# Performance work log

Measured on AMD Instinct MI355X. Metric: run time of the kernel, lower is better.

Reference implementation:

```python
import jax, jax.numpy as jnp
import numpy as np

N = 50000       # nodes
E = 800000      # edges (before self-loops)
F_IN = 128
HID = 64
HEADS = 4
OUT_DIM = 128
N_CLS = 2
NG = 500        # num graphs
SLOPE = 0.2     # GATConv leaky_relu negative slope
EPS = 1e-5      # BatchNorm eps


def setup_inputs() -> dict:
    key = jax.random.key(0)
    ks = jax.random.split(key, 24)
    s = 0.05
    d = {
        "x": jax.random.normal(ks[0], (N, F_IN), jnp.float32),
        "edge_index": jax.random.randint(ks[1], (2, E), 0, N, jnp.int64),
        "batch": jnp.sort(jax.random.randint(ks[2], (N,), 0, NG, jnp.int64)),
        # GATConv 1
        "W1": jax.random.normal(ks[3], (F_IN, HEADS * HID), jnp.float32) * s,
        "att_src1": jax.random.normal(ks[4], (HEADS, HID), jnp.float32) * s,
        "att_dst1": jax.random.normal(ks[5], (HEADS, HID), jnp.float32) * s,
        "b1": jnp.zeros((HEADS * HID,), jnp.float32),
        # BN1 (eval mode)
        "g1": jnp.ones((HEADS * HID,), jnp.float32),
        "be1": jnp.zeros((HEADS * HID,), jnp.float32),
        "rm1": jnp.zeros((HEADS * HID,), jnp.float32),
        "rv1": jnp.ones((HEADS * HID,), jnp.float32),
        # GATConv 2
        "W2": jax.random.normal(ks[6], (HEADS * HID, HEADS * HID), jnp.float32) * s,
        "att_src2": jax.random.normal(ks[7], (HEADS, HID), jnp.float32) * s,
        "att_dst2": jax.random.normal(ks[8], (HEADS, HID), jnp.float32) * s,
        "b2": jnp.zeros((HEADS * HID,), jnp.float32),
        # BN2 (eval mode)
        "g2": jnp.ones((HEADS * HID,), jnp.float32),
        "be2": jnp.zeros((HEADS * HID,), jnp.float32),
        "rm2": jnp.zeros((HEADS * HID,), jnp.float32),
        "rv2": jnp.ones((HEADS * HID,), jnp.float32),
        # MLP head
        "lw1": jax.random.normal(ks[9], (HEADS * HID, OUT_DIM), jnp.float32) * s,
        "lb1": jnp.zeros((OUT_DIM,), jnp.float32),
        "lw2": jax.random.normal(ks[10], (OUT_DIM, N_CLS), jnp.float32) * s,
        "lb2": jnp.zeros((N_CLS,), jnp.float32),
    }
    return d


def _gat_conv(x, src, dst, W, a_src, a_dst, b):
    """PyG GATConv (concat heads, add_self_loops=True, eval -> no dropout)."""
    n = x.shape[0]
    h = (x @ W).reshape(n, HEADS, -1)            # [N, H, C]
    loop = jnp.arange(n)
    s = jnp.concatenate([src, loop])             # self-loops appended
    d = jnp.concatenate([dst, loop])
    a_s = jnp.sum(h * a_src, axis=-1)            # [N, H]
    a_d = jnp.sum(h * a_dst, axis=-1)            # [N, H]
    e = jax.nn.leaky_relu(a_s[s] + a_d[d], SLOPE)   # [Et, H]
    # softmax over incoming edges per destination node
    m = jax.ops.segment_max(e, d, num_segments=n)
    ex = jnp.exp(e - m[d])
    denom = jax.ops.segment_sum(ex, d, num_segments=n)
    alpha = ex / denom[d]                        # [Et, H]
    msg = h[s] * alpha[:, :, None]               # [Et, H, C]
    out = jax.ops.segment_sum(msg, d, num_segments=n)
    return out.reshape(n, -1) + b


def _bn_eval(x, g, be, rm, rv):
    return (x - rm) * jax.lax.rsqrt(rv + EPS) * g + be


def reference(x, edge_index, batch, W1, att_src1, att_dst1, b1, g1, be1, rm1, rv1,
              W2, att_src2, att_dst2, b2, g2, be2, rm2, rv2, lw1, lb1, lw2, lb2):
    src, dst = edge_index[0], edge_index[1]
    h = jax.nn.relu(_gat_conv(x, src, dst, W1, att_src1, att_dst1, b1))
    h = _bn_eval(h, g1, be1, rm1, rv1)
    h = jax.nn.relu(_gat_conv(h, src, dst, W2, att_src2, att_dst2, b2))
    h = _bn_eval(h, g2, be2, rm2, rv2)
    # global mean pool over graphs
    sums = jax.ops.segment_sum(h, batch, num_segments=NG)
    cnt = jax.ops.segment_sum(jnp.ones((h.shape[0],), h.dtype), batch, num_segments=NG)
    pooled = sums / jnp.clip(cnt, 1.0)[:, None]
    z = jax.nn.relu(pooled @ lw1 + lb1)
    return z @ lw2 + lb2
```

## Files before the change

kernel.cpp:

```cpp
#include <hip/hip_runtime.h>
#include <hip/hip_bf16.h>
#include <math.h>

#define N_NODES 50000
#define M_PAD   50048
#define TILE_M  64
#define NBLK_GEMM (M_PAD / TILE_M)
#define NBLK_GEMM2 (M_PAD / 128)
#define NBLK_GAT (N_NODES / 4)
#define N_EDGES 800000
#define E8      (N_EDGES / 8)
#define NBLK_BUILD ((E8 + 255) / 256)
#define F_IN 128
#define HID 64
#define HEADS 4
#define FEAT 256
#define OUT_DIM 128
#define N_CLS 2
#define NG 500
#define SLOPE 0.2f
#define BN_EPS 1e-5f
#define ECAP 64

#define T_W1  (F_IN * 256)
#define T_W2  (FEAT * 256)
#define NBLK_W2T (T_W2 / 256)
#define HPAD_ULL ((M_PAD - N_NODES) * FEAT / 4)
#define POOLZ (NG * FEAT / 4)
#define PREP_THREADS (T_W1 + HPAD_ULL + N_NODES + POOLZ)
#define NBLK_PREP ((PREP_THREADS + 255) / 256)

typedef __attribute__((ext_vector_type(8))) short short8;
typedef __attribute__((ext_vector_type(4))) float floatx4;
typedef __attribute__((ext_vector_type(2))) float floatx2;

__device__ inline unsigned short f2bf(float f) {
    unsigned int u = __float_as_uint(f);
    unsigned int lsb = (u >> 16) & 1u;
    return (unsigned short)((u + 0x7fffu + lsb) >> 16);
}

__global__ __launch_bounds__(256) void prep_small(
    const float* __restrict__ W1, unsigned short* __restrict__ W1T,
    unsigned short* __restrict__ h1bf,
    int* __restrict__ deg, int* __restrict__ ell, int* __restrict__ ovf_cnt,
    float4* __restrict__ pooled4) {
    int gid = blockIdx.x * 256 + threadIdx.x;
    if (gid < T_W1) {
        int k = gid >> 8, n = gid & 255;
        W1T[n * F_IN + k] = f2bf(W1[gid]);
        return;
    }
    int j = gid - T_W1;
    if (j < HPAD_ULL) {
        ((unsigned long long*)(h1bf + (size_t)N_NODES * FEAT))[j] = 0ULL;
        return;
    }
    j -= HPAD_ULL;
    if (j < N_NODES) {
        deg[j] = 1;
        ell[(size_t)j * ECAP] = j;
        if (j == 0) *ovf_cnt = 0;
        return;
    }
    j -= N_NODES;
    if (j < POOLZ)
        pooled4[j] = make_float4(0.f, 0.f, 0.f, 0.f);
}

template<int K, bool AF32, int TM>
__device__ __forceinline__ void gemm_core(
    const void* __restrict__ Av, const unsigned short* __restrict__ BT,
    const float* __restrict__ att_src, const float* __restrict__ att_dst,
    unsigned char* __restrict__ h8, float* __restrict__ a_s,
    float* __restrict__ a_d, int bid, unsigned char* smem_raw) {
    constexpr int LS = 40;
    constexpr int C8 = 272;
    constexpr int MI = TM / 16;
    int t = threadIdx.x;
    unsigned short* As = (unsigned short*)smem_raw;
    unsigned short* Bs = As + TM * LS;
    unsigned char*  s8 = smem_raw;
    int lane = t & 63, w = t >> 6;
    int row0 = bid * TM;
    int mrow = lane & 15, quad = lane >> 4;

    floatx4 acc[MI][4] = {};

    int rA = t >> 2, cA = (t & 3) * 8;

    const unsigned short* Ab = (const unsigned short*)Av;
    const float* Af = (const float*)Av;

    for (int k0 = 0; k0 < K; k0 += 32) {
        #pragma unroll
        for (int j = 0; j < TM / 64; j++) {
            int r = rA + j * 64;
            if (AF32) {
                uint4 pk = make_uint4(0, 0, 0, 0);
                if (row0 + r < N_NODES) {
                    float4 f0 = *(const float4*)&Af[(long long)(row0 + r) * K + k0 + cA];
                    float4 f1 = *(const float4*)&Af[(long long)(row0 + r) * K + k0 + cA + 4];
                    pk.x = (unsigned)f2bf(f0.x) | ((unsigned)f2bf(f0.y) << 16);
                    pk.y = (unsigned)f2bf(f0.z) | ((unsigned)f2bf(f0.w) << 16);
                    pk.z = (unsigned)f2bf(f1.x) | ((unsigned)f2bf(f1.y) << 16);
                    pk.w = (unsigned)f2bf(f1.z) | ((unsigned)f2bf(f1.w) << 16);
                }
                *(uint4*)&As[r * LS + cA] = pk;
            } else {
                *(uint4*)&As[r * LS + cA] =
                    *(const uint4*)&Ab[(long long)(row0 + r) * K + k0 + cA];
            }
        }
        #pragma unroll
        for (int j = 0; j < 4; j++) {
            int r = rA + j * 64;
            *(uint4*)&Bs[r * LS + cA] = *(const uint4*)&BT[(long long)r * K + k0 + cA];
        }
        __syncthreads();
        short8 bf[4];
        #pragma unroll
        for (int ni = 0; ni < 4; ni++)
            bf[ni] = *(const short8*)&Bs[(w * 64 + ni * 16 + mrow) * LS + quad * 8];
        #pragma unroll
        for (int mi = 0; mi < MI; mi++) {
            short8 af = *(const short8*)&As[(mi * 16 + mrow) * LS + quad * 8];
            #pragma unroll
            for (int ni = 0; ni < 4; ni++)
                acc[mi][ni] = __builtin_amdgcn_mfma_f32_16x16x32_bf16(af, bf[ni],
                                                                      acc[mi][ni], 0, 0, 0);
        }
        __syncthreads();
    }

    float ats[4], atd[4];
    #pragma unroll
    for (int ni = 0; ni < 4; ni++) {
        ats[ni] = att_src[w * 64 + ni * 16 + mrow];
        atd[ni] = att_dst[w * 64 + ni * 16 + mrow];
    }
    #pragma unroll
    for (int mi = 0; mi < MI; mi++) {
        #pragma unroll
        for (int r = 0; r < 4; r++) {
            int row = row0 + mi * 16 + quad * 4 + r;
            float ps = 0.f, pd = 0.f;
            #pragma unroll
            for (int ni = 0; ni < 4; ni++) {
                float v = acc[mi][ni][r];
                ps += v * ats[ni];
                pd += v * atd[ni];
            }
            #pragma unroll
            for (int off = 1; off < 16; off <<= 1) {
                ps += __shfl_xor(ps, off);
                pd += __shfl_xor(pd, off);
            }
            if (mrow == 0 && row < N_NODES) {
                a_s[row * 4 + w] = ps;
                a_d[row * 4 + w] = pd;
            }
        }
    }

    #pragma unroll
    for (int mi = 0; mi < MI; mi++)
        #pragma unroll
        for (int r = 0; r < 4; r++) {
            int row = mi * 16 + quad * 4 + r;
            #pragma unroll
            for (int ni = 0; ni < 4; ni += 2) {
                int pk = __builtin_amdgcn_cvt_pk_fp8_f32(acc[mi][ni][r],
                                                         acc[mi][ni + 1][r], 0, false);
                s8[row * C8 + w * 64 + ni * 16 + mrow]       = (unsigned char)(pk & 0xff);
                s8[row * C8 + w * 64 + (ni + 1) * 16 + mrow] = (unsigned char)((pk >> 8) & 0xff);
            }
        }
    __syncthreads();
    if (TM == 64) {
        int r2 = t >> 2, q = t & 3;
        const uint4* sp = (const uint4*)&s8[r2 * C8 + q * 64];
        uint4* dp = (uint4*)&h8[(long long)(row0 + r2) * FEAT + q * 64];
        #pragma unroll
        for (int k = 0; k < 4; k++)
            dp[k] = sp[k];
    } else {
        int r2 = t >> 1, half = t & 1;
        const uint4* sp = (const uint4*)&s8[r2 * C8 + half * 128];
        uint4* dp = (uint4*)&h8[(long long)(row0 + r2) * FEAT + half * 128];
        #pragma unroll
        for (int k = 0; k < 8; k++)
            dp[k] = sp[k];
    }
}

__global__ __launch_bounds__(256, 4) void gemm1_build(
    const float* __restrict__ x, const unsigned short* __restrict__ BT,
    const float* __restrict__ W2, unsigned short* __restrict__ W2T,
    const float* __restrict__ att_src, const float* __restrict__ att_dst,
    unsigned char* __restrict__ h8, float* __restrict__ a_s,
    float* __restrict__ a_d,
    const int* __restrict__ src, const int* __restrict__ dst,
    int* __restrict__ deg, int* __restrict__ ell,
    int* __restrict__ ovf_cnt, int* __restrict__ ovf) {
    __shared__ __align__(16) unsigned char smem_raw[(TILE_M + FEAT) * 40 * 2];
    int bid = blockIdx.x;
    if (bid >= NBLK_GEMM + NBLK_W2T) {
        int i = (bid - NBLK_GEMM - NBLK_W2T) * 256 + threadIdx.x;
        if (i >= E8) return;
        int ss[8], dd[8], pp[8];
        #pragma unroll
        for (int j = 0; j < 8; j++) {
            ss[j] = src[i + j * E8];
            dd[j] = dst[i + j * E8];
        }
        #pragma unroll
        for (int j = 0; j < 8; j++)
            pp[j] = atomicAdd(&deg[dd[j]], 1);
        #pragma unroll
        for (int j = 0; j < 8; j++) {
            if (pp[j] < ECAP) {
                ell[(size_t)dd[j] * ECAP + pp[j]] = ss[j];
            } else {
                int k = atomicAdd(ovf_cnt, 1);
                ovf[2 * k] = ss[j]; ovf[2 * k + 1] = dd[j];
            }
        }
        return;
    }
    if (bid >= NBLK_GEMM) {
        int j = (bid - NBLK_GEMM) * 256 + threadIdx.x;
        int k = j >> 8, n = j & 255;
        W2T[n * FEAT + k] = f2bf(W2[j]);
        return;
    }
    gemm_core<F_IN, true, TILE_M>(x, BT, att_src, att_dst, h8, a_s, a_d,
                                  bid, smem_raw);
}

__global__ __launch_bounds__(256, 2) void gemm2k(
    const unsigned short* __restrict__ Ab, const unsigned short* __restrict__ BT,
    const float* __restrict__ att_src, const float* __restrict__ att_dst,
    unsigned char* __restrict__ h8, float* __restrict__ a_s,
    float* __restrict__ a_d) {
    __shared__ __align__(16) unsigned char smem_raw[128 * 272];
    gemm_core<FEAT, false, 128>(Ab, BT, att_src, att_dst, h8, a_s, a_d,
                                blockIdx.x, smem_raw);
}

template<bool POOL>
__device__ __forceinline__ void gat_core(
    const int* __restrict__ deg_arr, const int* __restrict__ ell,
    const int* __restrict__ ovf_cnt, const int* __restrict__ ovf,
    const float* __restrict__ a_s, const float* __restrict__ a_d,
    const unsigned char* __restrict__ h8, const float* __restrict__ bias,
    const float* __restrict__ g, const float* __restrict__ be,
    const float* __restrict__ rm, const float* __restrict__ rv,
    unsigned short* __restrict__ out16,
    const int* __restrict__ batch, float* __restrict__ pooled) {
    int t = threadIdx.x;
    int lane = t & 63;
    int w = t >> 6;
    int hd = lane >> 4;
    int d = blockIdx.x * 4 + w;

    __shared__ float p_lds[4 * ECAP * 4];
    __shared__ int   o_lds[4 * ECAP];
    __shared__ float4 shv[4][64];
    __shared__ int    shg[4];
    float* pw = &p_lds[w * ECAP * 4];
    int*   ow = &o_lds[w * ECAP];

    const unsigned int* __restrict__ H1 = (const unsigned int*)h8;

    int deg = deg_arr[d];
    float4 ad4 = *(const float4*)&a_d[d * 4];

    float den = 0.f;
    float4 acc = make_float4(0.f, 0.f, 0.f, 0.f);

    if (deg <= ECAP) {
        float lg[4] = {-INFINITY, -INFINITY, -INFINITY, -INFINITY};
        int s = 0;
        if (lane < deg) {
            s = ell[(size_t)d * ECAP + lane];
            float4 as4 = *(const float4*)&a_s[s * 4];
            float e0 = as4.x + ad4.x; lg[0] = e0 > 0.f ? e0 : SLOPE * e0;
            float e1 = as4.y + ad4.y; lg[1] = e1 > 0.f ? e1 : SLOPE * e1;
            float e2 = as4.z + ad4.z; lg[2] = e2 > 0.f ? e2 : SLOPE * e2;
            float e3 = as4.w + ad4.w; lg[3] = e3 > 0.f ? e3 : SLOPE * e3;
        }
        ow[lane] = s * 64;
        float mm = fmaxf(fmaxf(lg[0], lg[1]), fmaxf(lg[2], lg[3]));
        #pragma unroll
        for (int off = 1; off < 64; off <<= 1) mm = fmaxf(mm, __shfl_xor(mm, off));
        float4 pq = make_float4(0.f, 0.f, 0.f, 0.f);
        if (lane < deg) {
            pq.x = __expf(lg[0] - mm);
            pq.y = __expf(lg[1] - mm);
            pq.z = __expf(lg[2] - mm);
            pq.w = __expf(lg[3] - mm);
        }
        *(float4*)&pw[lane * 4] = pq;
        int deg4 = (deg + 3) & ~3;
        int cu[4];
        #pragma unroll
        for (int j = 0; j < 4; j++) cu[j] = (int)H1[ow[j] + lane];
        for (int e = 0; e < deg4; e += 4) {
            int nu[4] = {0, 0, 0, 0};
            if (e + 4 < deg4) {
                #pragma unroll
                for (int j = 0; j < 4; j++) nu[j] = (int)H1[ow[e + 4 + j] + lane];
            }
            #pragma unroll
            for (int j = 0; j < 4; j++) {
                float pj = pw[(e + j) * 4 + hd];
                den += pj;
                floatx2 lo = __builtin_amdgcn_cvt_pk_f32_fp8(cu[j], false);
                floatx2 hi = __builtin_amdgcn_cvt_pk_f32_fp8(cu[j], true);
                acc.x += pj * lo.x; acc.y += pj * lo.y;
                acc.z += pj * hi.x; acc.w += pj * hi.y;
            }
            #pragma unroll
            for (int j = 0; j < 4; j++) cu[j] = nu[j];
        }
    } else {
        float m_old;
        {
            int s = ell[(size_t)d * ECAP + lane];
            ow[lane] = s * 64;
            float4 as4 = *(const float4*)&a_s[s * 4];
            float lg[4];
            float e0 = as4.x + ad4.x; lg[0] = e0 > 0.f ? e0 : SLOPE * e0;
            float e1 = as4.y + ad4.y; lg[1] = e1 > 0.f ? e1 : SLOPE * e1;
            float e2 = as4.z + ad4.z; lg[2] = e2 > 0.f ? e2 : SLOPE * e2;
            float e3 = as4.w + ad4.w; lg[3] = e3 > 0.f ? e3 : SLOPE * e3;
            float mm = fmaxf(fmaxf(lg[0], lg[1]), fmaxf(lg[2], lg[3]));
            #pragma unroll
            for (int off = 1; off < 64; off <<= 1) mm = fmaxf(mm, __shfl_xor(mm, off));
            m_old = mm;
            float4 pq;
            pq.x = __expf(lg[0] - mm);
            pq.y = __expf(lg[1] - mm);
            pq.z = __expf(lg[2] - mm);
            pq.w = __expf(lg[3] - mm);
            *(float4*)&pw[lane * 4] = pq;
            for (int e = 0; e < ECAP; e++) {
                int oA = ow[e];
                float pA = pw[e * 4 + hd];
                int uA = (int)H1[oA + lane];
                den += pA;
                floatx2 a0 = __builtin_amdgcn_cvt_pk_f32_fp8(uA, false);
                floatx2 a1 = __builtin_amdgcn_cvt_pk_f32_fp8(uA, true);
                acc.x += pA * a0.x; acc.y += pA * a0.y;
                acc.z += pA * a1.x; acc.w += pA * a1.y;
            }
        }
        int nov = *ovf_cnt;
        for (int i = 0; i < nov; i++) {
            int s2 = ovf[2 * i], d2 = ovf[2 * i + 1];
            if (d2 != d) continue;
            float4 as4 = *(const float4*)&a_s[s2 * 4];
            float lg[4];
            float e0 = as4.x + ad4.x; lg[0] = e0 > 0.f ? e0 : SLOPE * e0;
            float e1 = as4.y + ad4.y; lg[1] = e1 > 0.f ? e1 : SLOPE * e1;
            float e2 = as4.z + ad4.z; lg[2] = e2 > 0.f ? e2 : SLOPE * e2;
            float e3 = as4.w + ad4.w; lg[3] = e3 > 0.f ? e3 : SLOPE * e3;
            float mmax = fmaxf(fmaxf(lg[0], lg[1]), fmaxf(lg[2], lg[3]));
            float m_new = fmaxf(m_old, mmax);
            float alpha = __expf(m_old - m_new);
            m_old = m_new;
            float ph = __expf(lg[hd] - m_new);
            acc.x *= alpha; acc.y *= alpha; acc.z *= alpha; acc.w *= alpha;
            den = den * alpha + ph;
            int u = (int)H1[s2 * 64 + lane];
            floatx2 a0 = __builtin_amdgcn_cvt_pk_f32_fp8(u, false);
            floatx2 a1 = __builtin_amdgcn_cvt_pk_f32_fp8(u, true);
            acc.x += ph * a0.x; acc.y += ph * a0.y;
            acc.z += ph * a1.x; acc.w += ph * a1.y;
        }
    }
    float inv = 1.f / den;
    int c0 = lane * 4;
    float4 bi = *(const float4*)&bias[c0];
    float4 gg = *(const float4*)&g[c0];
    float4 bb = *(const float4*)&be[c0];
    float4 mm4 = *(const float4*)&rm[c0];
    float4 vv = *(const float4*)&rv[c0];
    float v0 = fmaxf(acc.x * inv + bi.x, 0.f);
    float v1 = fmaxf(acc.y * inv + bi.y, 0.f);
    float v2 = fmaxf(acc.z * inv + bi.z, 0.f);
    float v3 = fmaxf(acc.w * inv + bi.w, 0.f);
    v0 = (v0 - mm4.x) * rsqrtf(vv.x + BN_EPS) * gg.x + bb.x;
    v1 = (v1 - mm4.y) * rsqrtf(vv.y + BN_EPS) * gg.y + bb.y;
    v2 = (v2 - mm4.z) * rsqrtf(vv.z + BN_EPS) * gg.z + bb.z;
    v3 = (v3 - mm4.w) * rsqrtf(vv.w + BN_EPS) * gg.w + bb.w;
    if (!POOL) {
        unsigned long long o =
            (unsigned long long)f2bf(v0) |
            ((unsigned long long)f2bf(v1) << 16) |
            ((unsigned long long)f2bf(v2) << 32) |
            ((unsigned long long)f2bf(v3) << 48);
        __builtin_nontemporal_store(o, (unsigned long long*)&out16[(long long)d * FEAT + c0]);
    } else {
        shv[w][lane] = make_float4(v0, v1, v2, v3);
        if (lane == 0) shg[w] = (int)batch[d];
        __syncthreads();
        int cl = t >> 2, ce = t & 3;
        float r0 = ((const float*)&shv[0][cl])[ce];
        float r1 = ((const float*)&shv[1][cl])[ce];
        float r2 = ((const float*)&shv[2][cl])[ce];
        float r3 = ((const float*)&shv[3][cl])[ce];
        int g0 = shg[0], g1 = shg[1], g2 = shg[2], g3 = shg[3];
        if (g0 == g3) {
            atomicAdd(&pooled[g0 * FEAT + t], r0 + r1 + r2 + r3);
        } else {
            float sum = r0;
            int gp = g0;
            if (g1 == gp) sum += r1; else { atomicAdd(&pooled[gp * FEAT + t], sum); gp = g1; sum = r1; }
            if (g2 == gp) sum += r2; else { atomicAdd(&pooled[gp * FEAT + t], sum); gp = g2; sum = r2; }
            if (g3 == gp) sum += r3; else { atomicAdd(&pooled[gp * FEAT + t], sum); gp = g3; sum = r3; }
            atomicAdd(&pooled[gp * FEAT + t], sum);
        }
    }
}

__global__ __launch_bounds__(256) void gat1(
    const int* __restrict__ deg_arr, const int* __restrict__ ell,
    const int* __restrict__ ovf_cnt, const int* __restrict__ ovf,
    const float* __restrict__ a_s, const float* __restrict__ a_d,
    const unsigned char* __restrict__ h8, const float* __restrict__ bias,
    const float* __restrict__ g, const float* __restrict__ be,
    const float* __restrict__ rm, const float* __restrict__ rv,
    unsigned short* __restrict__ out16) {
    gat_core<false>(deg_arr, ell, ovf_cnt, ovf, a_s, a_d, h8, bias, g, be,
                    rm, rv, out16, nullptr, nullptr);
}

__global__ __launch_bounds__(256) void gat2_pool(
    const int* __restrict__ deg_arr, const int* __restrict__ ell,
    const int* __restrict__ ovf_cnt, const int* __restrict__ ovf,
    const float* __restrict__ a_s, const float* __restrict__ a_d,
    const unsigned char* __restrict__ h8, const float* __restrict__ bias,
    const float* __restrict__ g, const float* __restrict__ be,
    const float* __restrict__ rm, const float* __restrict__ rv,
    const int* __restrict__ batch, float* __restrict__ pooled) {
    gat_core<true>(deg_arr, ell, ovf_cnt, ovf, a_s, a_d, h8, bias, g, be,
                   rm, rv, nullptr, batch, pooled);
}

__global__ __launch_bounds__(256) void head_mlp(
    const float* __restrict__ pooled, const int* __restrict__ batch,
    const float* __restrict__ lw1, const float* __restrict__ lb1,
    const float* __restrict__ lw2, const float* __restrict__ lb2,
    float* __restrict__ out) {
    int gph = blockIdx.x;
    int t = threadIdx.x;
    __shared__ float pl[FEAT];
    __shared__ float zl[OUT_DIM];
    __shared__ int lo_s, hi_s;
    if (t == 0) {
        int lo = 0, hi = N_NODES;
        while (lo < hi) { int mid = (lo + hi) >> 1; if (batch[mid] < gph) lo = mid + 1; else hi = mid; }
        lo_s = lo;
        int lo2 = 0, hi2 = N_NODES;
        while (lo2 < hi2) { int mid = (lo2 + hi2) >> 1; if (batch[mid] < gph + 1) lo2 = mid + 1; else hi2 = mid; }
        hi_s = lo2;
    }
    __syncthreads();
    float cnt = fmaxf((float)(hi_s - lo_s), 1.f);
    pl[t] = pooled[gph * FEAT + t] / cnt;
    __syncthreads();
    int j = t >> 1, kh = t & 1;
    float zp = 0.f;
    #pragma unroll 8
    for (int k = kh * 128; k < kh * 128 + 128; k++)
        zp += pl[k] * lw1[k * OUT_DIM + j];
    zp += __shfl_xor(zp, 1);
    if (kh == 0) zl[j] = fmaxf(zp + lb1[j], 0.f);
    __syncthreads();
    int w = t >> 6, lane = t & 63;
    if (w < 2) {
        float p = zl[lane] * lw2[lane * 2 + w] + zl[lane + 64] * lw2[(lane + 64) * 2 + w];
        #pragma unroll
        for (int off = 1; off < 64; off <<= 1) p += __shfl_xor(p, off);
        if (lane == 0) out[gph * 2 + w] = p + lb2[w];
    }
}

extern "C" void kernel_launch(void* const* d_in, const int* in_sizes, int n_in,
                              void* d_out, int out_size, void* d_ws, size_t ws_size,
                              hipStream_t stream) {
    const float* x       = (const float*)d_in[0];
    const int*   ei      = (const int*)d_in[1];
    const int*   batch   = (const int*)d_in[2];
    const float* W1      = (const float*)d_in[3];
    const float* att_s1  = (const float*)d_in[4];
    const float* att_d1  = (const float*)d_in[5];
    const float* b1      = (const float*)d_in[6];
    const float* g1      = (const float*)d_in[7];
    const float* be1     = (const float*)d_in[8];
    const float* rm1     = (const float*)d_in[9];
    const float* rv1     = (const float*)d_in[10];
    const float* W2      = (const float*)d_in[11];
    const float* att_s2  = (const float*)d_in[12];
    const float* att_d2  = (const float*)d_in[13];
    const float* b2      = (const float*)d_in[14];
    const float* g2      = (const float*)d_in[15];
    const float* be2     = (const float*)d_in[16];
    const float* rm2     = (const float*)d_in[17];
    const float* rv2     = (const float*)d_in[18];
    const float* lw1     = (const float*)d_in[19];
    const float* lb1     = (const float*)d_in[20];
    const float* lw2     = (const float*)d_in[21];
    const float* lb2     = (const float*)d_in[22];
    float* out           = (float*)d_out;

    const int* src = ei;
    const int* dst = ei + N_EDGES;

    char* p = (char*)d_ws;
    auto carve = [&p](size_t bytes) -> void* {
        void* r = (void*)p;
        p += (bytes + 63) & ~(size_t)63;
        return r;
    };
    float* pooled = (float*)carve(sizeof(float) * NG * FEAT);
    float* a_s    = (float*)carve(sizeof(float) * N_NODES * HEADS);
    float* a_d    = (float*)carve(sizeof(float) * N_NODES * HEADS);
    int*   deg    = (int*)carve(sizeof(int) * N_NODES);
    int*   ovf_cnt= (int*)carve(sizeof(int) * 16);
    int*   ell    = (int*)carve(sizeof(int) * (size_t)N_NODES * ECAP);
    int*   ovf    = (int*)carve(sizeof(int) * 2 * (N_EDGES + N_NODES));
    unsigned char*  h8   = (unsigned char*)carve((size_t)M_PAD * FEAT);
    unsigned short* h1bf = (unsigned short*)carve(sizeof(short) * (size_t)M_PAD * FEAT);
    unsigned short* w1t  = (unsigned short*)carve(sizeof(short) * FEAT * F_IN);
    unsigned short* w2t  = (unsigned short*)carve(sizeof(short) * FEAT * FEAT);

    prep_small<<<NBLK_PREP, 256, 0, stream>>>(W1, w1t, h1bf, deg, ell, ovf_cnt,
                                              (float4*)pooled);

    gemm1_build<<<NBLK_GEMM + NBLK_W2T + NBLK_BUILD, 256, 0, stream>>>(
        x, w1t, W2, w2t, att_s1, att_d1, h8, a_s, a_d,
        src, dst, deg, ell, ovf_cnt, ovf);
    gat1<<<NBLK_GAT, 256, 0, stream>>>(deg, ell, ovf_cnt, ovf, a_s, a_d, h8,
                                       b1, g1, be1, rm1, rv1, h1bf);

    gemm2k<<<NBLK_GEMM2, 256, 0, stream>>>(
        h1bf, w2t, att_s2, att_d2, h8, a_s, a_d);
    gat2_pool<<<NBLK_GAT, 256, 0, stream>>>(deg, ell, ovf_cnt, ovf, a_s, a_d,
                                            h8, b2, g2, be2, rm2, rv2,
                                            batch, pooled);

    head_mlp<<<NG, 256, 0, stream>>>(pooled, batch, lw1, lb1, lw2, lb2, out);
}
```

Before: 287.1 us.

## Build ELL adjacency via two-pass binning by destination block in LDS

Replaces direct per-node global atomics and scattered ELL writes with a two-pass build. Edges are first binned into 64-node buckets using a coarse atomic counter and packed (src<<6 | local dst) records. A new kernel then builds each bucket's ELL rows in shared memory and writes them out with coalesced int4 stores. The aim is to cut global atomic contention and random scatter, at the cost of an extra kernel launch, a bin buffer, and full ELL tile writes.

Result: slower. 448.2 us (+56.1%).

```diff
diff --git a/kernel.cpp b/kernel.cpp
--- a/kernel.cpp
+++ b/kernel.cpp
@@ -10,7 +10,9 @@
 #define NBLK_GAT (N_NODES / 4)
 #define N_EDGES 800000
 #define E8      (N_EDGES / 8)
-#define NBLK_BUILD ((E8 + 255) / 256)
+#define NBLK_BINA ((E8 + 255) / 256)
+#define NBINS   NBLK_GEMM
+#define BINCAP  1280
 #define F_IN 128
 #define HID 64
 #define HEADS 4
@@ -27,7 +29,7 @@
 #define NBLK_W2T (T_W2 / 256)
 #define HPAD_ULL ((M_PAD - N_NODES) * FEAT / 4)
 #define POOLZ (NG * FEAT / 4)
-#define PREP_THREADS (T_W1 + HPAD_ULL + N_NODES + POOLZ)
+#define PREP_THREADS (T_W1 + HPAD_ULL + POOLZ + NBINS)
 #define NBLK_PREP ((PREP_THREADS + 255) / 256)
 
 typedef __attribute__((ext_vector_type(8))) short short8;
@@ -43,8 +45,8 @@
 __global__ __launch_bounds__(256) void prep_small(
     const float* __restrict__ W1, unsigned short* __restrict__ W1T,
     unsigned short* __restrict__ h1bf,
-    int* __restrict__ deg, int* __restrict__ ell, int* __restrict__ ovf_cnt,
-    float4* __restrict__ pooled4) {
+    float4* __restrict__ pooled4, int* __restrict__ bin_cnt,
+    int* __restrict__ ovf_cnt) {
     int gid = blockIdx.x * 256 + threadIdx.x;
     if (gid < T_W1) {
         int k = gid >> 8, n = gid & 255;
@@ -57,15 +59,15 @@
         return;
     }
     j -= HPAD_ULL;
-    if (j < N_NODES) {
-        deg[j] = 1;
-        ell[(size_t)j * ECAP] = j;
+    if (j < POOLZ) {
+        pooled4[j] = make_float4(0.f, 0.f, 0.f, 0.f);
+        return;
+    }
+    j -= POOLZ;
+    if (j < NBINS) {
+        bin_cnt[j] = 0;
         if (j == 0) *ovf_cnt = 0;
-        return;
-    }
-    j -= N_NODES;
-    if (j < POOLZ)
-        pooled4[j] = make_float4(0.f, 0.f, 0.f, 0.f);
+    }
 }
 
 template<int K, bool AF32, int TM>
@@ -201,7 +203,7 @@
     unsigned char* __restrict__ h8, float* __restrict__ a_s,
     float* __restrict__ a_d,
     const int* __restrict__ src, const int* __restrict__ dst,
-    int* __restrict__ deg, int* __restrict__ ell,
+    unsigned* __restrict__ bins, int* __restrict__ bin_cnt,
     int* __restrict__ ovf_cnt, int* __restrict__ ovf) {
     __shared__ __align__(16) unsigned char smem_raw[(TILE_M + FEAT) * 40 * 2];
     int bid = blockIdx.x;
@@ -216,11 +218,12 @@
         }
         #pragma unroll
         for (int j = 0; j < 8; j++)
-            pp[j] = atomicAdd(&deg[dd[j]], 1);
+            pp[j] = atomicAdd(&bin_cnt[dd[j] >> 6], 1);
         #pragma unroll
         for (int j = 0; j < 8; j++) {
-            if (pp[j] < ECAP) {
-                ell[(size_t)dd[j] * ECAP + pp[j]] = ss[j];
+            if (pp[j] < BINCAP) {
+                bins[(size_t)(dd[j] >> 6) * BINCAP + pp[j]] =
+                    ((unsigned)ss[j] << 6) | (unsigned)(dd[j] & 63);
             } else {
                 int k = atomicAdd(ovf_cnt, 1);
                 ovf[2 * k] = ss[j]; ovf[2 * k + 1] = dd[j];
@@ -236,6 +239,44 @@
     }
     gemm_core<F_IN, true, TILE_M>(x, BT, att_src, att_dst, h8, a_s, a_d,
                                   bid, smem_raw);
+}
+
+__global__ __launch_bounds__(256) void bin_ell(
+    const unsigned* __restrict__ bins, const int* __restrict__ bin_cnt,
+    int* __restrict__ deg, int* __restrict__ ell,
+    int* __restrict__ ovf_cnt, int* __restrict__ ovf) {
+    __shared__ int ell_lds[64 * ECAP];
+    __shared__ int deg_lds[64];
+    int b = blockIdx.x;
+    int t = threadIdx.x;
+    int base = b * 64;
+    if (t < 64) {
+        deg_lds[t] = 1;
+        ell_lds[t * ECAP] = base + t;
+    }
+    __syncthreads();
+    int cnt = bin_cnt[b];
+    if (cnt > BINCAP) cnt = BINCAP;
+    for (int r = t; r < cnt; r += 256) {
+        unsigned rec = bins[(size_t)b * BINCAP + r];
+        int n = rec & 63;
+        int s = (int)(rec >> 6);
+        int pos = atomicAdd(&deg_lds[n], 1);
+        if (pos < ECAP) {
+            ell_lds[n * ECAP + pos] = s;
+        } else {
+            int k = atomicAdd(ovf_cnt, 1);
+            ovf[2 * k] = s; ovf[2 * k + 1] = base + n;
+        }
+    }
+    __syncthreads();
+    if (t < 64 && base + t < N_NODES) deg[base + t] = deg_lds[t];
+    const int4* el = (const int4*)ell_lds;
+    int4* eg = (int4*)&ell[(size_t)base * ECAP];
+    for (int q = t; q < 64 * ECAP / 4; q += 256) {
+        int node = base + (q >> 4);
+        if (node < N_NODES) eg[q] = el[q];
+    }
 }
 
 __global__ __launch_bounds__(256, 2) void gemm2k(
@@ -532,17 +573,22 @@
     int*   ovf_cnt= (int*)carve(sizeof(int) * 16);
     int*   ell    = (int*)carve(sizeof(int) * (size_t)N_NODES * ECAP);
     int*   ovf    = (int*)carve(sizeof(int) * 2 * (N_EDGES + N_NODES));
+    unsigned* bins= (unsigned*)carve(sizeof(unsigned) * (size_t)NBINS * BINCAP);
+    int* bin_cnt  = (int*)carve(sizeof(int) * NBINS);
     unsigned char*  h8   = (unsigned char*)carve((size_t)M_PAD * FEAT);
     unsigned short* h1bf = (unsigned short*)carve(sizeof(short) * (size_t)M_PAD * FEAT);
     unsigned short* w1t  = (unsigned short*)carve(sizeof(short) * FEAT * F_IN);
     unsigned short* w2t  = (unsigned short*)carve(sizeof(short) * FEAT * FEAT);
 
-    prep_small<<<NBLK_PREP, 256, 0, stream>>>(W1, w1t, h1bf, deg, ell, ovf_cnt,
-                                              (float4*)pooled);
-
-    gemm1_build<<<NBLK_GEMM + NBLK_W2T + NBLK_BUILD, 256, 0, stream>>>(
+    prep_small<<<NBLK_PREP, 256, 0, stream>>>(W1, w1t, h1bf, (float4*)pooled,
+                                              bin_cnt, ovf_cnt);
+
+    gemm1_build<<<NBLK_GEMM + NBLK_W2T + NBLK_BINA, 256, 0, stream>>>(
         x, w1t, W2, w2t, att_s1, att_d1, h8, a_s, a_d,
-        src, dst, deg, ell, ovf_cnt, ovf);
+        src, dst, bins, bin_cnt, ovf_cnt, ovf);
+
+    bin_ell<<<NBINS, 256, 0, stream>>>(bins, bin_cnt, deg, ell, ovf_cnt, ovf);
+
     gat1<<<NBLK_GAT, 256, 0, stream>>>(deg, ell, ovf_cnt, ovf, a_s, a_d, h8,
                                        b1, g1, be1, rm1, rv1, h1bf);
 
```
